# Kernel optimization log

Hardware: AMD Instinct MI355X
Metric: run time of the kernel (lower is better)

## Reference

```python
import jax, jax.numpy as jnp
import numpy as np

N, E = 65536, 524288
IN_DIM, HID_DIM, OUT_DIM = 1024, 512, 256


def setup_inputs() -> dict:
    key = jax.random.key(0)
    k1, k2, k3, k4, k5, k6 = jax.random.split(key, 6)
    h = jax.random.normal(k1, (N, IN_DIM), dtype=jnp.float32)
    src = jax.random.randint(k2, (E,), 0, N, dtype=jnp.int64)
    dst = jax.random.randint(k3, (E,), 0, N, dtype=jnp.int64)
    # Glorot-uniform weights as in DGL GraphConv
    lim1 = float(np.sqrt(6.0 / (IN_DIM + HID_DIM)))
    lim2 = float(np.sqrt(6.0 / (HID_DIM + OUT_DIM)))
    W1 = jax.random.uniform(k4, (IN_DIM, HID_DIM), jnp.float32, -lim1, lim1)
    W2 = jax.random.uniform(k5, (HID_DIM, OUT_DIM), jnp.float32, -lim2, lim2)
    b1 = jnp.zeros((HID_DIM,), jnp.float32)
    b2 = jnp.zeros((OUT_DIM,), jnp.float32)
    return {"h": h, "W1": W1, "b1": b1, "W2": W2, "b2": b2, "src": src, "dst": dst}


def _graph_conv(x, W, b, src, dst, inv_sqrt_dout, inv_sqrt_din):
    # DGL GraphConv, norm='both': D_in^{-1/2} A D_out^{-1/2} X W + b
    # Apply dense transform first (in_dim >= out_dim path in DGL) -- same math.
    x = x * inv_sqrt_dout[:, None]
    x = x @ W  # [N, out]
    agg = jax.ops.segment_sum(x[src], dst, num_segments=x.shape[0])  # scatter-add over edges
    return agg * inv_sqrt_din[:, None] + b


def reference(h, W1, b1, W2, b2, src, dst):
    n = h.shape[0]
    ones = jnp.ones((src.shape[0],), h.dtype)
    deg_out = jnp.maximum(jax.ops.segment_sum(ones, src, num_segments=n), 1.0)
    deg_in = jnp.maximum(jax.ops.segment_sum(ones, dst, num_segments=n), 1.0)
    inv_sqrt_dout = jax.lax.rsqrt(deg_out)
    inv_sqrt_din = jax.lax.rsqrt(deg_in)
    x = _graph_conv(h, W1, b1, src, dst, inv_sqrt_dout, inv_sqrt_din)
    x = jax.nn.elu(x)  # act; dropout p=0 -> identity
    out = _graph_conv(x, W2, b2, src, dst, inv_sqrt_dout, inv_sqrt_din)
    return out  # last_act = Identity
```

## Files before the change

### kernel.cpp

```cpp
#include <hip/hip_runtime.h>
#include <hip/hip_bf16.h>

#define IN_DIM 1024
#define HID 512
#define OUTD 256

typedef __attribute__((ext_vector_type(8))) short short8;
typedef __attribute__((ext_vector_type(4))) float f32x4;
typedef __attribute__((ext_vector_type(8))) unsigned short ushort8e;
typedef __attribute__((ext_vector_type(4))) unsigned short ushort4e;

template<int F> struct VecSel;
template<> struct VecSel<8> { using T = ushort8e; };
template<> struct VecSel<4> { using T = ushort4e; };


__device__ inline unsigned short f2bf(float f) {
    union { float f; unsigned u; } v; v.f = f;
    unsigned r = (v.u + 0x7FFF + ((v.u >> 16) & 1)) >> 16;
    return (unsigned short)r;
}

__device__ inline float bf2f(unsigned short u) {
    union { unsigned u; float f; } v; v.u = ((unsigned)u) << 16; return v.f;
}

__device__ inline void gload16(const void* g, void* l) {
    __builtin_amdgcn_global_load_lds(
        (const __attribute__((address_space(1))) void*)g,
        (__attribute__((address_space(3))) void*)l, 16, 0, 0);
}


__global__ void deg_kernel(const int* __restrict__ src, const int* __restrict__ dst,
                           int* __restrict__ dego, int* __restrict__ degi, int E) {
    int i = blockIdx.x * blockDim.x + threadIdx.x;
    if (i < E) {
        atomicAdd(&dego[src[i]], 1);
        atomicAdd(&degi[dst[i]], 1);
    }
}

__global__ void invsqrt_kernel(const int* __restrict__ dego, const int* __restrict__ degi,
                               float* __restrict__ iso, float* __restrict__ isi, int n) {
    int i = blockIdx.x * blockDim.x + threadIdx.x;
    if (i < n) {
        iso[i] = rsqrtf(fmaxf((float)dego[i], 1.0f));
        isi[i] = rsqrtf(fmaxf((float)degi[i], 1.0f));
    }
}


__global__ __launch_bounds__(256) void scan_block(const int* __restrict__ deg,
                                                  int* __restrict__ excl,
                                                  int* __restrict__ partials) {
    __shared__ int tmp[256];
    int tid = threadIdx.x;
    int i = blockIdx.x * 256 + tid;
    int v = deg[i];
    tmp[tid] = v;
    __syncthreads();
    #pragma unroll
    for (int off = 1; off < 256; off <<= 1) {
        int t = (tid >= off) ? tmp[tid - off] : 0;
        __syncthreads();
        tmp[tid] += t;
        __syncthreads();
    }
    excl[i] = tmp[tid] - v;
    if (tid == 255) partials[blockIdx.x] = tmp[255];
}

__global__ __launch_bounds__(256) void scan_partials(int* __restrict__ partials) {
    __shared__ int tmp[256];
    int tid = threadIdx.x;
    int v = partials[tid];
    tmp[tid] = v;
    __syncthreads();
    #pragma unroll
    for (int off = 1; off < 256; off <<= 1) {
        int t = (tid >= off) ? tmp[tid - off] : 0;
        __syncthreads();
        tmp[tid] += t;
        __syncthreads();
    }
    partials[tid] = tmp[tid] - v;
}

__global__ __launch_bounds__(256) void scan_add(const int* __restrict__ excl,
                                                const int* __restrict__ partials,
                                                const int* __restrict__ deg,
                                                int* __restrict__ row_start,
                                                int* __restrict__ cursor, int n) {
    int i = blockIdx.x * 256 + threadIdx.x;
    int v = excl[i] + partials[blockIdx.x];
    row_start[i] = v;
    cursor[i] = v;
    if (i == n - 1) row_start[n] = v + deg[i];
}

__global__ void csr_fill(const int* __restrict__ src, const int* __restrict__ dst,
                         int* __restrict__ cursor, int* __restrict__ eidx, int E) {
    int e = blockIdx.x * blockDim.x + threadIdx.x;
    if (e < E) {
        int pos = atomicAdd(&cursor[dst[e]], 1);
        eidx[pos] = src[e];
    }
}


__global__ __launch_bounds__(256) void scale_cvt(
    const float* __restrict__ x, const float* __restrict__ rs,
    unsigned short* __restrict__ y, int logK, size_t total)
{
    size_t i = ((size_t)blockIdx.x * 256 + threadIdx.x) * 8;
    if (i >= total) return;
    float s = rs[i >> logK];
    float4 a = *reinterpret_cast<const float4*>(x + i);
    float4 b = *reinterpret_cast<const float4*>(x + i + 4);
    short8 o;
    o[0] = (short)f2bf(a.x * s); o[1] = (short)f2bf(a.y * s);
    o[2] = (short)f2bf(a.z * s); o[3] = (short)f2bf(a.w * s);
    o[4] = (short)f2bf(b.x * s); o[5] = (short)f2bf(b.y * s);
    o[6] = (short)f2bf(b.z * s); o[7] = (short)f2bf(b.w * s);
    *reinterpret_cast<short8*>(y + i) = o;
}

__global__ void transpose_cvt(const float* __restrict__ W, unsigned short* __restrict__ Wt,
                              int K, int N) {
    int i = blockIdx.x * 256 + threadIdx.x;
    if (i < N * K) {
        int n = i / K, k = i - n * K;
        Wt[i] = f2bf(W[(size_t)k * N + n]);
    }
}


#define TM 128
#define TN 128
#define TK 32

__global__ __launch_bounds__(256) void gemm_bf16_mfma(
    const unsigned short* __restrict__ A,
    const unsigned short* __restrict__ Bt,
    unsigned short* __restrict__ Cb,
    int M, int K, int Nc)
{
    __shared__ unsigned short As[TM][TK];
    __shared__ unsigned short Bs[TN][TK];

    const int tid  = threadIdx.x;
    const int lane = tid & 63;
    const int wave = tid >> 6;
    const int wr = wave >> 1, wc = wave & 1;
    const int lrow = lane & 15;
    const int lkg  = lane >> 4;

    const int m0 = blockIdx.y * TM;
    const int n0 = blockIdx.x * TN;

    const int s0 = wave * 64 + lane;
    const int s1 = s0 + 256;
    const int r0 = s0 >> 2, q0 = (s0 & 3) ^ ((s0 >> 3) & 3);
    const int r1 = s1 >> 2, q1 = (s1 & 3) ^ ((s1 >> 3) & 3);

    char* AsB = (char*)&As[0][0];
    char* BsB = (char*)&Bs[0][0];
    void* ldsA0 = AsB + wave * 1024;
    void* ldsA1 = AsB + 4096 + wave * 1024;
    void* ldsB0 = BsB + wave * 1024;
    void* ldsB1 = BsB + 4096 + wave * 1024;

    const int rslot = (lkg ^ ((lrow >> 1) & 3)) * 8;

    f32x4 acc[4][4] = {};

    const int nk = K / TK;
    for (int kt = 0; kt < nk; ++kt) {
        const int k0 = kt * TK;
        gload16(A  + (size_t)(m0 + r0) * K + k0 + q0 * 8, ldsA0);
        gload16(A  + (size_t)(m0 + r1) * K + k0 + q1 * 8, ldsA1);
        gload16(Bt + (size_t)(n0 + r0) * K + k0 + q0 * 8, ldsB0);
        gload16(Bt + (size_t)(n0 + r1) * K + k0 + q1 * 8, ldsB1);
        __syncthreads();

        short8 af[4], bfr[4];
        #pragma unroll
        for (int mi = 0; mi < 4; ++mi)
            af[mi] = *reinterpret_cast<const short8*>(&As[wr * 64 + mi * 16 + lrow][rslot]);
        #pragma unroll
        for (int ni = 0; ni < 4; ++ni)
            bfr[ni] = *reinterpret_cast<const short8*>(&Bs[wc * 64 + ni * 16 + lrow][rslot]);

        #pragma unroll
        for (int mi = 0; mi < 4; ++mi)
            #pragma unroll
            for (int ni = 0; ni < 4; ++ni)
                acc[mi][ni] = __builtin_amdgcn_mfma_f32_16x16x32_bf16(
                    af[mi], bfr[ni], acc[mi][ni], 0, 0, 0);

        __syncthreads();
    }

    #pragma unroll
    for (int mi = 0; mi < 4; ++mi)
        #pragma unroll
        for (int ni = 0; ni < 4; ++ni)
            #pragma unroll
            for (int r = 0; r < 4; ++r)
                Cb[(size_t)(m0 + wr * 64 + mi * 16 + lkg * 4 + r) * Nc
                   + (n0 + wc * 64 + ni * 16 + lrow)] = f2bf(acc[mi][ni][r]);
}


template<int DIM, bool LAYER1>
__global__ __launch_bounds__(256) void aggregate(
    const int* __restrict__ row_start, const int* __restrict__ eidx,
    const unsigned short* __restrict__ Xb, const float* __restrict__ isi,
    const float* __restrict__ iso, const float* __restrict__ bias,
    unsigned short* __restrict__ out_bf, float* __restrict__ out_f)
{
    constexpr int F = DIM / 64;
    using VecT = typename VecSel<F>::T;
    const int node = blockIdx.x * 4 + (threadIdx.x >> 6);
    const int lane = threadIdx.x & 63;

    const int beg = row_start[node];
    const int end = row_start[node + 1];
    const unsigned short* base = Xb + lane * F;

    float acc[F] = {};
    int e = beg;
    for (; e + 1 < end; e += 2) {
        int i0 = eidx[e], i1 = eidx[e + 1];
        VecT v0 = *reinterpret_cast<const VecT*>(base + (size_t)i0 * DIM);
        VecT v1 = *reinterpret_cast<const VecT*>(base + (size_t)i1 * DIM);
        #pragma unroll
        for (int f = 0; f < F; ++f) { acc[f] += bf2f(v0[f]); acc[f] += bf2f(v1[f]); }
    }
    if (e < end) {
        VecT v0 = *reinterpret_cast<const VecT*>(base + (size_t)eidx[e] * DIM);
        #pragma unroll
        for (int f = 0; f < F; ++f) acc[f] += bf2f(v0[f]);
    }

    const float si = isi[node];
    float bv[F];
    #pragma unroll
    for (int q = 0; q < F / 4; ++q)
        *reinterpret_cast<float4*>(&bv[q * 4]) =
            *reinterpret_cast<const float4*>(bias + lane * F + q * 4);

    if (LAYER1) {
        const float so = iso[node];
        short8 o;
        #pragma unroll
        for (int f = 0; f < F; ++f) {
            float v = acc[f] * si + bv[f];
            v = v > 0.f ? v : expm1f(v);
            o[f] = (short)f2bf(v * so);
        }
        *reinterpret_cast<short8*>(out_bf + (size_t)node * DIM + lane * F) = o;
    } else {
        #pragma unroll
        for (int q = 0; q < F / 4; ++q) {
            float4 v = make_float4(acc[q * 4 + 0] * si + bv[q * 4 + 0],
                                   acc[q * 4 + 1] * si + bv[q * 4 + 1],
                                   acc[q * 4 + 2] * si + bv[q * 4 + 2],
                                   acc[q * 4 + 3] * si + bv[q * 4 + 3]);
            *reinterpret_cast<float4*>(out_f + (size_t)node * DIM + lane * F + q * 4) = v;
        }
    }
}


extern "C" void kernel_launch(void* const* d_in, const int* in_sizes, int n_in,
                              void* d_out, int out_size, void* d_ws, size_t ws_size,
                              hipStream_t stream) {
    const float* h  = (const float*)d_in[0];
    const float* W1 = (const float*)d_in[1];
    const float* b1 = (const float*)d_in[2];
    const float* W2 = (const float*)d_in[3];
    const float* b2 = (const float*)d_in[4];
    const int*   src = (const int*)d_in[5];
    const int*   dst = (const int*)d_in[6];

    const int N = in_sizes[0] / IN_DIM;
    const int E = in_sizes[5];
    float* out = (float*)d_out;

    int* dego      = (int*)d_ws;
    int* degi      = dego + N;
    int* excl      = degi + N;
    int* partials  = excl + N;
    int* row_start = partials + 256;
    int* cursor    = row_start + N + 64;
    int* eidx      = cursor + N;
    float* iso     = (float*)(eidx + E);
    float* isi     = iso + N;
    unsigned short* W1t = (unsigned short*)(isi + N);
    unsigned short* W2t = W1t + (size_t)IN_DIM * HID;
    unsigned short* hb  = W2t + (size_t)HID * OUTD;
    unsigned short* X1b = hb + (size_t)N * IN_DIM;
    unsigned short* X2b = X1b;
    unsigned short* R2h = X1b + (size_t)N * HID;

    hipMemsetAsync(dego, 0, sizeof(int) * (size_t)2 * N, stream);

    deg_kernel<<<(E + 255) / 256, 256, 0, stream>>>(src, dst, dego, degi, E);
    invsqrt_kernel<<<(N + 255) / 256, 256, 0, stream>>>(dego, degi, iso, isi, N);

    scan_block<<<N / 256, 256, 0, stream>>>(degi, excl, partials);
    scan_partials<<<1, 256, 0, stream>>>(partials);
    scan_add<<<N / 256, 256, 0, stream>>>(excl, partials, degi, row_start, cursor, N);
    csr_fill<<<(E + 255) / 256, 256, 0, stream>>>(src, dst, cursor, eidx, E);

    scale_cvt<<<(unsigned)(((size_t)N * IN_DIM / 8 + 255) / 256), 256, 0, stream>>>(
        h, iso, hb, 10, (size_t)N * IN_DIM);
    transpose_cvt<<<(IN_DIM * HID + 255) / 256, 256, 0, stream>>>(W1, W1t, IN_DIM, HID);
    transpose_cvt<<<(HID * OUTD + 255) / 256, 256, 0, stream>>>(W2, W2t, HID, OUTD);

    dim3 g1(HID / TN, N / TM);
    gemm_bf16_mfma<<<g1, 256, 0, stream>>>(hb, W1t, X1b, N, IN_DIM, HID);
    aggregate<HID, true><<<N / 4, 256, 0, stream>>>(
        row_start, eidx, X1b, isi, iso, b1, R2h, nullptr);

    dim3 g2(OUTD / TN, N / TM);
    gemm_bf16_mfma<<<g2, 256, 0, stream>>>(R2h, W2t, X2b, N, HID, OUTD);
    aggregate<OUTD, false><<<N / 4, 256, 0, stream>>>(
        row_start, eidx, X2b, isi, iso, b2, nullptr, out);
}
```

Baseline: 438.5 us.

## Remap GEMM blocks across XCDs, grid-stride conversion, unroll aggregation by four

```diff
diff --git a/kernel.cpp b/kernel.cpp
--- a/kernel.cpp
+++ b/kernel.cpp
@@ -113,17 +113,18 @@
     const float* __restrict__ x, const float* __restrict__ rs,
     unsigned short* __restrict__ y, int logK, size_t total)
 {
-    size_t i = ((size_t)blockIdx.x * 256 + threadIdx.x) * 8;
-    if (i >= total) return;
-    float s = rs[i >> logK];
-    float4 a = *reinterpret_cast<const float4*>(x + i);
-    float4 b = *reinterpret_cast<const float4*>(x + i + 4);
-    short8 o;
-    o[0] = (short)f2bf(a.x * s); o[1] = (short)f2bf(a.y * s);
-    o[2] = (short)f2bf(a.z * s); o[3] = (short)f2bf(a.w * s);
-    o[4] = (short)f2bf(b.x * s); o[5] = (short)f2bf(b.y * s);
-    o[6] = (short)f2bf(b.z * s); o[7] = (short)f2bf(b.w * s);
-    *reinterpret_cast<short8*>(y + i) = o;
+    const size_t stride = (size_t)gridDim.x * 256 * 8;
+    for (size_t i = ((size_t)blockIdx.x * 256 + threadIdx.x) * 8; i < total; i += stride) {
+        float s = rs[i >> logK];
+        float4 a = *reinterpret_cast<const float4*>(x + i);
+        float4 b = *reinterpret_cast<const float4*>(x + i + 4);
+        short8 o;
+        o[0] = (short)f2bf(a.x * s); o[1] = (short)f2bf(a.y * s);
+        o[2] = (short)f2bf(a.z * s); o[3] = (short)f2bf(a.w * s);
+        o[4] = (short)f2bf(b.x * s); o[5] = (short)f2bf(b.y * s);
+        o[6] = (short)f2bf(b.z * s); o[7] = (short)f2bf(b.w * s);
+        *reinterpret_cast<short8*>(y + i) = o;
+    }
 }
 
 __global__ void transpose_cvt(const float* __restrict__ W, unsigned short* __restrict__ Wt,
@@ -139,6 +140,7 @@
 #define TM 128
 #define TN 128
 #define TK 32
+#define NXCD 8
 
 __global__ __launch_bounds__(256) void gemm_bf16_mfma(
     const unsigned short* __restrict__ A,
@@ -156,8 +158,13 @@
     const int lrow = lane & 15;
     const int lkg  = lane >> 4;
 
-    const int m0 = blockIdx.y * TM;
-    const int n0 = blockIdx.x * TN;
+    const int nwg = gridDim.x;
+    const int per = nwg / NXCD;
+    const int lin = blockIdx.x;
+    const int newlin = (lin % NXCD) * per + lin / NXCD;
+    const int ncb = Nc / TN;
+    const int m0 = (newlin / ncb) * TM;
+    const int n0 = (newlin % ncb) * TN;
 
     const int s0 = wave * 64 + lane;
     const int s1 = s0 + 256;
@@ -231,14 +238,19 @@
 
     float acc[F] = {};
     int e = beg;
-    for (; e + 1 < end; e += 2) {
-        int i0 = eidx[e], i1 = eidx[e + 1];
+    for (; e + 3 < end; e += 4) {
+        int i0 = eidx[e], i1 = eidx[e + 1], i2 = eidx[e + 2], i3 = eidx[e + 3];
         VecT v0 = *reinterpret_cast<const VecT*>(base + (size_t)i0 * DIM);
         VecT v1 = *reinterpret_cast<const VecT*>(base + (size_t)i1 * DIM);
-        #pragma unroll
-        for (int f = 0; f < F; ++f) { acc[f] += bf2f(v0[f]); acc[f] += bf2f(v1[f]); }
-    }
-    if (e < end) {
+        VecT v2 = *reinterpret_cast<const VecT*>(base + (size_t)i2 * DIM);
+        VecT v3 = *reinterpret_cast<const VecT*>(base + (size_t)i3 * DIM);
+        #pragma unroll
+        for (int f = 0; f < F; ++f) {
+            acc[f] += bf2f(v0[f]); acc[f] += bf2f(v1[f]);
+            acc[f] += bf2f(v2[f]); acc[f] += bf2f(v3[f]);
+        }
+    }
+    for (; e < end; ++e) {
         VecT v0 = *reinterpret_cast<const VecT*>(base + (size_t)eidx[e] * DIM);
         #pragma unroll
         for (int f = 0; f < F; ++f) acc[f] += bf2f(v0[f]);
@@ -315,18 +327,17 @@
     scan_add<<<N / 256, 256, 0, stream>>>(excl, partials, degi, row_start, cursor, N);
     csr_fill<<<(E + 255) / 256, 256, 0, stream>>>(src, dst, cursor, eidx, E);
 
-    scale_cvt<<<(unsigned)(((size_t)N * IN_DIM / 8 + 255) / 256), 256, 0, stream>>>(
-        h, iso, hb, 10, (size_t)N * IN_DIM);
+    scale_cvt<<<2048, 256, 0, stream>>>(h, iso, hb, 10, (size_t)N * IN_DIM);
     transpose_cvt<<<(IN_DIM * HID + 255) / 256, 256, 0, stream>>>(W1, W1t, IN_DIM, HID);
     transpose_cvt<<<(HID * OUTD + 255) / 256, 256, 0, stream>>>(W2, W2t, HID, OUTD);
 
-    dim3 g1(HID / TN, N / TM);
-    gemm_bf16_mfma<<<g1, 256, 0, stream>>>(hb, W1t, X1b, N, IN_DIM, HID);
+    gemm_bf16_mfma<<<(N / TM) * (HID / TN), 256, 0, stream>>>(
+        hb, W1t, X1b, N, IN_DIM, HID);
     aggregate<HID, true><<<N / 4, 256, 0, stream>>>(
         row_start, eidx, X1b, isi, iso, b1, R2h, nullptr);
 
-    dim3 g2(OUTD / TN, N / TM);
-    gemm_bf16_mfma<<<g2, 256, 0, stream>>>(R2h, W2t, X2b, N, HID, OUTD);
+    gemm_bf16_mfma<<<(N / TM) * (OUTD / TN), 256, 0, stream>>>(
+        R2h, W2t, X2b, N, HID, OUTD);
     aggregate<OUTD, false><<<N / 4, 256, 0, stream>>>(
         row_start, eidx, X2b, isi, iso, b2, nullptr, out);
 }
```

Result: no change. 443.2 us (+1.1%).
